# Performance work log

Measured on AMD Instinct MI355X. Metric: run time of the kernel, lower is better.

The kernel has to match this reference:

```python
import jax, jax.numpy as jnp
import numpy as np

B, T, D, H, FF, TB = 4, 512, 768, 12, 3072, 64
DK = D // H
E = float(np.e)
NEG = -1e9  # stand-in for float('-inf') masked_fill; rows always have valid entries


def layer_norm(x, g, b, eps=1e-5):
    m = jnp.mean(x, axis=-1, keepdims=True)
    v = jnp.mean((x - m) ** 2, axis=-1, keepdims=True)
    return (x - m) * jax.lax.rsqrt(v + eps) * g + b


def setup_inputs() -> dict:
    key = jax.random.key(0)
    ks = jax.random.split(key, 20)
    s = 0.02
    w = lambda k, shape: jax.random.normal(k, shape, jnp.float32) * s
    return {
        "x": jax.random.normal(ks[0], (B, T, D), jnp.float32),
        "batch_temporal_mat": jax.random.uniform(ks[1], (B, T, T), jnp.float32, 0.0, 100.0),
        "padding_masks": jnp.ones((B, 1, T, T), jnp.int32),
        # attention linears (stored (in,out): y = x @ W + b, equals torch x @ W_t.T + b)
        "wq": w(ks[2], (D, D)), "bq": w(ks[3], (D,)),
        "wk": w(ks[4], (D, D)), "bk": w(ks[5], (D,)),
        "wv": w(ks[6], (D, D)), "bv": w(ks[7], (D,)),
        "wp": w(ks[8], (D, D)), "bp": w(ks[9], (D,)),
        # temporal-bias MLP: Linear(1,TB) -> leaky_relu(0.2) -> Linear(TB,1)
        "tb1_w": w(ks[10], (1, TB)), "tb1_b": w(ks[11], (TB,)),
        "tb2_w": w(ks[12], (TB, 1)), "tb2_b": w(ks[13], (1,)),
        # FFN
        "fc1_w": w(ks[14], (D, FF)), "fc1_b": w(ks[15], (FF,)),
        "fc2_w": w(ks[16], (FF, D)), "fc2_b": w(ks[17], (D,)),
        # layernorms
        "ln1_g": jnp.ones((D,), jnp.float32), "ln1_b": jnp.zeros((D,), jnp.float32),
        "ln2_g": jnp.ones((D,), jnp.float32), "ln2_b": jnp.zeros((D,), jnp.float32),
    }


def _block(x, batch_temporal_mat, padding_masks,
           wq, bq, wk, bk, wv, bv, wp, bp,
           tb1_w, tb1_b, tb2_w, tb2_b,
           fc1_w, fc1_b, fc2_w, fc2_b,
           ln1_g, ln1_b, ln2_g, ln2_b):
    # pre-LN attention sublayer
    h = layer_norm(x, ln1_g, ln1_b)
    q = (h @ wq + bq).reshape(B, T, H, DK).transpose(0, 2, 1, 3)  # (B,H,T,DK)
    k = (h @ wk + bk).reshape(B, T, H, DK).transpose(0, 2, 1, 3)
    v = (h @ wv + bv).reshape(B, T, H, DK).transpose(0, 2, 1, 3)
    scores = jnp.einsum('bhid,bhjd->bhij', q, k) * (DK ** -0.5)  # (B,H,T,T)

    # temporal bias: 1/log(e + dt), then per-(i,j) MLP with leaky_relu(0.2)
    tm = 1.0 / jnp.log(E + batch_temporal_mat)                    # (B,T,T)
    hb = jax.nn.leaky_relu(tm[..., None] @ tb1_w + tb1_b, 0.2)    # (B,T,T,TB)
    bias = (hb @ tb2_w + tb2_b)[..., 0]                           # (B,T,T)
    scores = scores + bias[:, None]

    # padding mask then causal (future) mask with CLS row 0 fully visible
    scores = jnp.where(padding_masks == 0, NEG, scores)
    causal = jnp.triu(jnp.ones((T, T), bool), 1).at[0, :].set(False)
    scores = jnp.where(causal, NEG, scores)

    p = jax.nn.softmax(scores, axis=-1)
    out = jnp.einsum('bhij,bhjd->bhid', p, v).transpose(0, 2, 1, 3).reshape(B, T, D)
    out = out @ wp + bp
    x = x + out

    # pre-LN FFN sublayer (exact GELU as in nn.GELU default)
    h2 = layer_norm(x, ln2_g, ln2_b)
    m = jax.nn.gelu(h2 @ fc1_w + fc1_b, approximate=False) @ fc2_w + fc2_b
    return x + m


def reference(x, batch_temporal_mat, padding_masks,
              wq, bq, wk, bk, wv, bv, wp, bp,
              tb1_w, tb1_b, tb2_w, tb2_b,
              fc1_w, fc1_b, fc2_w, fc2_b,
              ln1_g, ln1_b, ln2_g, ln2_b):
    return _block(x, batch_temporal_mat, padding_masks,
                  wq, bq, wk, bk, wv, bv, wp, bp,
                  tb1_w, tb1_b, tb2_w, tb2_b,
                  fc1_w, fc1_b, fc2_w, fc2_b,
                  ln1_g, ln1_b, ln2_g, ln2_b)
```

## Files before the change

kernel.cpp:

```cpp
#include <hip/hip_runtime.h>
#include <hip/hip_bf16.h>
#include <math.h>

#define B_ 4
#define T_ 512
#define D_ 768
#define H_ 12
#define FF_ 3072
#define DK_ 64
#define NTOK (B_*T_)
#define NEGV -1e9f

typedef unsigned short u16;
typedef __bf16 bfx8 __attribute__((ext_vector_type(8)));
typedef float f32x4 __attribute__((ext_vector_type(4)));
typedef u16 u16x8 __attribute__((ext_vector_type(8)));

__device__ __forceinline__ u16 f2bf(float f) {
  union { float f; unsigned u; } v; v.f = f;
  unsigned r = (v.u + 0x7FFFu + ((v.u >> 16) & 1u)) >> 16;
  return (u16)r;
}

__device__ __forceinline__ void glds16(const u16* g, u16* l) {
  __builtin_amdgcn_global_load_lds((const __attribute__((address_space(1))) void*)g,
                                   (__attribute__((address_space(3))) void*)l, 16, 0, 0);
}

__global__ __launch_bounds__(256) void prep_kernel(
    const float* __restrict__ x,
    const float* __restrict__ wq, const float* __restrict__ wk,
    const float* __restrict__ wv, const float* __restrict__ wp,
    const float* __restrict__ fc1, const float* __restrict__ fc2,
    u16* wqT, u16* wkT, u16* wvT, u16* wpT, u16* fc1T, u16* fc2T,
    const float* __restrict__ ln1g, const float* __restrict__ ln1b, u16* __restrict__ hbuf,
    const float* __restrict__ tmat, const int* __restrict__ pad,
    const float* __restrict__ tb1w, const float* __restrict__ tb1b,
    const float* __restrict__ tb2w, const float* __restrict__ tb2b,
    float* __restrict__ biasM)
{
  const int bid = blockIdx.x;
  const int tid = threadIdx.x;
  if (bid < 6912) {
    __shared__ float tile[32][33];
    const float* in; u16* outp; int K, N, local;
    if (bid < 2304) {
      int m = bid / 576; local = bid % 576; K = 768; N = 768;
      in   = m == 0 ? wq  : (m == 1 ? wk  : (m == 2 ? wv  : wp));
      outp = m == 0 ? wqT : (m == 1 ? wkT : (m == 2 ? wvT : wpT));
    } else if (bid < 4608) {
      local = bid - 2304; K = 768; N = 3072; in = fc1; outp = fc1T;
    } else {
      local = bid - 4608; K = 3072; N = 768; in = fc2; outp = fc2T;
    }
    const int nt = N / 32;
    const int n0 = (local % nt) * 32, k0 = (local / nt) * 32;
    const int tx = tid & 31, ty = tid >> 5;
    #pragma unroll
    for (int i = 0; i < 4; ++i) {
      int r = ty + i * 8;
      tile[r][tx] = in[(size_t)(k0 + r) * N + n0 + tx];
    }
    __syncthreads();
    #pragma unroll
    for (int i = 0; i < 4; ++i) {
      int r = ty + i * 8;
      outp[(size_t)(n0 + r) * K + k0 + tx] = f2bf(tile[tx][r]);
    }
  } else if (bid < 8960) {
    const int row = bid - 6912;
    const float* xr = x + (size_t)row * D_;
    float v0 = xr[tid], v1 = xr[tid + 256], v2 = xr[tid + 512];
    float s = v0 + v1 + v2;
    float sq = v0 * v0 + v1 * v1 + v2 * v2;
    #pragma unroll
    for (int o = 32; o > 0; o >>= 1) { s += __shfl_down(s, o); sq += __shfl_down(sq, o); }
    __shared__ float ss[4], s2[4];
    int w = tid >> 6;
    if ((tid & 63) == 0) { ss[w] = s; s2[w] = sq; }
    __syncthreads();
    s = ss[0] + ss[1] + ss[2] + ss[3];
    sq = s2[0] + s2[1] + s2[2] + s2[3];
    float mean = s * (1.0f / 768.0f);
    float inv = rsqrtf(sq * (1.0f / 768.0f) - mean * mean + 1e-5f);
    u16* orow = hbuf + (size_t)row * D_;
    orow[tid]       = f2bf((v0 - mean) * inv * ln1g[tid]       + ln1b[tid]);
    orow[tid + 256] = f2bf((v1 - mean) * inv * ln1g[tid + 256] + ln1b[tid + 256]);
    orow[tid + 512] = f2bf((v2 - mean) * inv * ln1g[tid + 512] + ln1b[tid + 512]);
  } else {
    __shared__ float sw1[64], sb1[64], sw2[64];
    if (tid < 64) {
      sw1[tid] = tb1w[tid];
      sb1[tid] = tb1b[tid];
      sw2[tid] = tb2w[tid];
    }
    __syncthreads();
    size_t idx = (size_t)(bid - 8960) * 256 + tid;
    float tm = 1.0f / __logf(2.718281828459045f + tmat[idx]);
    float acc = tb2b[0];
    #pragma unroll
    for (int t = 0; t < 64; ++t) {
      float u = fmaf(tm, sw1[t], sb1[t]);
      u = u > 0.0f ? u : 0.2f * u;
      acc = fmaf(u, sw2[t], acc);
    }
    biasM[idx] = (pad[idx] == 0) ? NEGV : acc;
  }
}

__device__ __forceinline__ void gemm_tile_p2(
    const u16* __restrict__ A, const u16* __restrict__ BT,
    int K, int nk, int m0, int n0,
    u16* As, u16* Bs, f32x4 acc[4][4])
{
  const int tid = threadIdx.x;
  const int w = tid >> 6, lane = tid & 63;
  const int lr = lane & 15, lk = (lane >> 4) * 8;
  const int wm = (w >> 1) * 64, wn = (w & 1) * 64;
  const int c0 = w * 64 + lane, c1 = 256 + c0;
  const int r0 = c0 >> 2, o0 = (c0 & 3) * 8;
  const int r1 = c1 >> 2, o1 = (c1 & 3) * 8;
  const u16* gA0 = A  + (size_t)(m0 + r0) * K + o0;
  const u16* gA1 = A  + (size_t)(m0 + r1) * K + o1;
  const u16* gB0 = BT + (size_t)(n0 + r0) * K + o0;
  const u16* gB1 = BT + (size_t)(n0 + r1) * K + o1;
  u16* la0 = As + w * 512;
  u16* la1 = As + 2048 + w * 512;
  u16* lb0 = Bs + w * 512;
  u16* lb1 = Bs + 2048 + w * 512;
#define ISSUE_TILE(kk, b) do { \
    glds16(gA0 + (size_t)(kk) * 32, la0 + (b) * 4096); \
    glds16(gA1 + (size_t)(kk) * 32, la1 + (b) * 4096); \
    glds16(gB0 + (size_t)(kk) * 32, lb0 + (b) * 4096); \
    glds16(gB1 + (size_t)(kk) * 32, lb1 + (b) * 4096); } while (0)
  ISSUE_TILE(0, 0);
  if (nk > 1) ISSUE_TILE(1, 1);
  int cb = 0;
  for (int kt = 0; kt < nk; ++kt) {
    if (kt < nk - 2) asm volatile("s_waitcnt vmcnt(4)" ::: "memory");
    else             asm volatile("s_waitcnt vmcnt(0)" ::: "memory");
    __builtin_amdgcn_sched_barrier(0);
    __builtin_amdgcn_s_barrier();
    __builtin_amdgcn_sched_barrier(0);
    const u16* Asc = As + cb * 4096;
    const u16* Bsc = Bs + cb * 4096;
    bfx8 af[4], bfr[4];
    #pragma unroll
    for (int t = 0; t < 4; ++t) {
      af[t]  = *(const bfx8*)&Asc[(wm + t * 16 + lr) * 32 + lk];
      bfr[t] = *(const bfx8*)&Bsc[(wn + t * 16 + lr) * 32 + lk];
    }
    #pragma unroll
    for (int rt = 0; rt < 4; ++rt)
      #pragma unroll
      for (int ct = 0; ct < 4; ++ct)
        acc[rt][ct] = __builtin_amdgcn_mfma_f32_16x16x32_bf16(af[rt], bfr[ct], acc[rt][ct], 0, 0, 0);
    if (kt + 2 < nk) {
      int nb = cb + 2; if (nb >= 3) nb -= 3;
      ISSUE_TILE(kt + 2, nb);
    }
    cb = cb + 1; if (cb >= 3) cb = 0;
  }
#undef ISSUE_TILE
}

__global__ __launch_bounds__(256) void gemm_qkv(
    const u16* __restrict__ A,
    const u16* __restrict__ wqT, const u16* __restrict__ wkT, const u16* __restrict__ wvT,
    const float* __restrict__ bq, const float* __restrict__ bk, const float* __restrict__ bv,
    u16* __restrict__ qo, u16* __restrict__ ko, u16* __restrict__ vo)
{
  __shared__ u16 As[3 * 128 * 32];
  __shared__ u16 Bs[3 * 128 * 32];
  const int z = blockIdx.z;
  const u16* BT = z == 0 ? wqT : (z == 1 ? wkT : wvT);
  const float* bias = z == 0 ? bq : (z == 1 ? bk : bv);
  u16* outp = z == 0 ? qo : (z == 1 ? ko : vo);
  const float scale = z == 0 ? 0.125f : 1.0f;
  const int m0 = blockIdx.y * 128, n0 = blockIdx.x * 128;
  f32x4 acc[4][4];
  #pragma unroll
  for (int a = 0; a < 4; ++a)
    #pragma unroll
    for (int bb = 0; bb < 4; ++bb) acc[a][bb] = (f32x4){0.f, 0.f, 0.f, 0.f};
  gemm_tile_p2(A, BT, D_, D_ / 32, m0, n0, As, Bs, acc);
  const int tid = threadIdx.x;
  const int w = tid >> 6, lane = tid & 63;
  const int lr = lane & 15;
  const int wm = (w >> 1) * 64, wn = (w & 1) * 64;
  #pragma unroll
  for (int rt = 0; rt < 4; ++rt)
    #pragma unroll
    for (int ct = 0; ct < 4; ++ct)
      #pragma unroll
      for (int r = 0; r < 4; ++r) {
        int m = m0 + wm + rt * 16 + (lane >> 4) * 4 + r;
        int n = n0 + wn + ct * 16 + lr;
        float val = (acc[rt][ct][r] + bias[n]) * scale;
        int b = m >> 9, t = m & 511, hh = n >> 6, d = n & 63;
        if (z < 2) outp[(((size_t)b * H_ + hh) * T_ + t) * DK_ + d] = f2bf(val);
        else       outp[(((size_t)b * H_ + hh) * DK_ + d) * T_ + t] = f2bf(val);
      }
}

__global__ __launch_bounds__(256) void gemm_res(
    const u16* __restrict__ A, const u16* __restrict__ BT,
    const float* __restrict__ bias, const float* __restrict__ resid,
    float* __restrict__ outp, int K)
{
  __shared__ u16 As[3 * 128 * 32];
  __shared__ u16 Bs[3 * 64 * 32];
  const int bid = blockIdx.x;
  const int xcd = bid & 7, i = bid >> 3;
  const int mt = xcd * 2 + (i >= 12 ? 1 : 0);
  const int nt = i - (i >= 12 ? 12 : 0);
  const int m0 = mt * 128, n0 = nt * 64;
  const int nk = K / 32;

  const int tid = threadIdx.x;
  const int w = tid >> 6, lane = tid & 63;
  const int lr = lane & 15, hi = lane >> 4, lk = hi * 8;
  const int wm = (w >> 1) * 64, wn = (w & 1) * 32;
  const int c0 = w * 64 + lane, c1 = 256 + c0;
  const int rA0 = c0 >> 2, oA0 = (c0 & 3) * 8;
  const int rA1 = c1 >> 2, oA1 = (c1 & 3) * 8;
  const int rB  = c0 >> 2, oB  = (c0 & 3) * 8;
  const u16* gA0 = A  + (size_t)(m0 + rA0) * K + oA0;
  const u16* gA1 = A  + (size_t)(m0 + rA1) * K + oA1;
  const u16* gB  = BT + (size_t)(n0 + rB) * K + oB;
  u16* la0 = As + w * 512;
  u16* la1 = As + 2048 + w * 512;
  u16* lb  = Bs + w * 512;

  f32x4 acc[4][2];
  #pragma unroll
  for (int a = 0; a < 4; ++a)
    #pragma unroll
    for (int bb = 0; bb < 2; ++bb) acc[a][bb] = (f32x4){0.f, 0.f, 0.f, 0.f};

#define ISSUE_T(kk, b) do { \
    glds16(gA0 + (size_t)(kk) * 32, la0 + (b) * 4096); \
    glds16(gA1 + (size_t)(kk) * 32, la1 + (b) * 4096); \
    glds16(gB  + (size_t)(kk) * 32, lb  + (b) * 2048); } while (0)
  ISSUE_T(0, 0);
  if (nk > 1) ISSUE_T(1, 1);
  int cb = 0;
  for (int kt = 0; kt < nk; ++kt) {
    if (kt < nk - 2) asm volatile("s_waitcnt vmcnt(3)" ::: "memory");
    else             asm volatile("s_waitcnt vmcnt(0)" ::: "memory");
    __builtin_amdgcn_sched_barrier(0);
    __builtin_amdgcn_s_barrier();
    __builtin_amdgcn_sched_barrier(0);
    const u16* Asc = As + cb * 4096;
    const u16* Bsc = Bs + cb * 2048;
    bfx8 af[4], bfr[2];
    #pragma unroll
    for (int t = 0; t < 4; ++t)
      af[t] = *(const bfx8*)&Asc[(wm + t * 16 + lr) * 32 + lk];
    #pragma unroll
    for (int u = 0; u < 2; ++u)
      bfr[u] = *(const bfx8*)&Bsc[(wn + u * 16 + lr) * 32 + lk];
    #pragma unroll
    for (int rt = 0; rt < 4; ++rt)
      #pragma unroll
      for (int ct = 0; ct < 2; ++ct)
        acc[rt][ct] = __builtin_amdgcn_mfma_f32_16x16x32_bf16(af[rt], bfr[ct], acc[rt][ct], 0, 0, 0);
    if (kt + 2 < nk) {
      int nb = cb + 2; if (nb >= 3) nb -= 3;
      ISSUE_T(kt + 2, nb);
    }
    cb = cb + 1; if (cb >= 3) cb = 0;
  }
#undef ISSUE_T

  #pragma unroll
  for (int rt = 0; rt < 4; ++rt)
    #pragma unroll
    for (int ct = 0; ct < 2; ++ct)
      #pragma unroll
      for (int r = 0; r < 4; ++r) {
        int m = m0 + wm + rt * 16 + hi * 4 + r;
        int n = n0 + wn + ct * 16 + lr;
        size_t off = (size_t)m * D_ + n;
        outp[off] = acc[rt][ct][r] + bias[n] + resid[off];
      }
}

__global__ __launch_bounds__(256) void gemm_gelu(
    const u16* __restrict__ A, const u16* __restrict__ BT,
    const float* __restrict__ bias, u16* __restrict__ outp, int M, int N, int K)
{
  __shared__ u16 As[3 * 128 * 32];
  __shared__ u16 Bs[3 * 128 * 32];
  const int m0 = blockIdx.y * 128, n0 = blockIdx.x * 128;
  f32x4 acc[4][4];
  #pragma unroll
  for (int a = 0; a < 4; ++a)
    #pragma unroll
    for (int bb = 0; bb < 4; ++bb) acc[a][bb] = (f32x4){0.f, 0.f, 0.f, 0.f};
  gemm_tile_p2(A, BT, K, K / 32, m0, n0, As, Bs, acc);
  const int tid = threadIdx.x;
  const int w = tid >> 6, lane = tid & 63;
  const int lr = lane & 15;
  const int wm = (w >> 1) * 64, wn = (w & 1) * 64;
  #pragma unroll
  for (int rt = 0; rt < 4; ++rt)
    #pragma unroll
    for (int ct = 0; ct < 4; ++ct)
      #pragma unroll
      for (int r = 0; r < 4; ++r) {
        int m = m0 + wm + rt * 16 + (lane >> 4) * 4 + r;
        int n = n0 + wn + ct * 16 + lr;
        float val = acc[rt][ct][r] + bias[n];
        float gl = 0.5f * val * (1.0f + erff(val * 0.7071067811865475f));
        outp[(size_t)m * N + n] = f2bf(gl);
      }
}

__global__ __launch_bounds__(256) void ln2_kernel(
    const float* __restrict__ x1, const float* __restrict__ g, const float* __restrict__ bta,
    u16* __restrict__ h2)
{
  const int row = blockIdx.x;
  const int tid = threadIdx.x;
  const size_t base = (size_t)row * D_;
  float v[3];
  float s = 0.f, sq = 0.f;
  #pragma unroll
  for (int i = 0; i < 3; ++i) {
    int c = tid + i * 256;
    float val = x1[base + c];
    v[i] = val;
    s += val; sq += val * val;
  }
  #pragma unroll
  for (int o = 32; o > 0; o >>= 1) { s += __shfl_down(s, o); sq += __shfl_down(sq, o); }
  __shared__ float ss[4], s2[4];
  int w = tid >> 6;
  if ((tid & 63) == 0) { ss[w] = s; s2[w] = sq; }
  __syncthreads();
  s = ss[0] + ss[1] + ss[2] + ss[3];
  sq = s2[0] + s2[1] + s2[2] + s2[3];
  float mean = s * (1.0f / 768.0f);
  float inv = rsqrtf(sq * (1.0f / 768.0f) - mean * mean + 1e-5f);
  #pragma unroll
  for (int i = 0; i < 3; ++i) {
    int c = tid + i * 256;
    h2[base + c] = f2bf((v[i] - mean) * inv * g[c] + bta[c]);
  }
}

__global__ __launch_bounds__(256) void attn_kernel(
    const u16* __restrict__ q, const u16* __restrict__ k, const u16* __restrict__ vT,
    const float* __restrict__ biasM, u16* __restrict__ ao)
{
  __shared__ u16 P[32 * 512];
  __shared__ float pmax[128], psum[128];
  const int tid = threadIdx.x;
  const int w = tid >> 6, lane = tid & 63;
  const int lr = lane & 15, hi = lane >> 4, lk = hi * 8;

  const int bid = blockIdx.x;
  const int xcd = bid & 7, idx = bid >> 3;
  const int bh = xcd * 6 + (idx >> 4);
  const int i0 = (idx & 15) * 32;
  const int b = bh / H_, h = bh % H_;
  const int tmax = (i0 == 0) ? 31 : ((i0 >> 4) + 1);
  const int nks  = (i0 == 0) ? 16 : ((i0 >> 5) + 1);

  bfx8 qf[2][2];
  #pragma unroll
  for (int g = 0; g < 2; ++g)
    #pragma unroll
    for (int ks = 0; ks < 2; ++ks)
      qf[g][ks] = *(const bfx8*)(q + ((size_t)bh * T_ + i0 + g * 16 + lr) * DK_ + ks * 32 + lk);
  f32x4 acc[8][2];
  float mx[2][4];
  #pragma unroll
  for (int g = 0; g < 2; ++g)
    #pragma unroll
    for (int r = 0; r < 4; ++r) mx[g][r] = -3.4e38f;
  #pragma unroll
  for (int ct = 0; ct < 8; ++ct) {
    const int t = ct * 4 + w;
    if (t > tmax) continue;
    const int j0 = t * 16;
    bfx8 kf0 = *(const bfx8*)(k + ((size_t)bh * T_ + j0 + lr) * DK_ + lk);
    bfx8 kf1 = *(const bfx8*)(k + ((size_t)bh * T_ + j0 + lr) * DK_ + 32 + lk);
    const int j = j0 + lr;
    #pragma unroll
    for (int g = 0; g < 2; ++g) {
      f32x4 a0 = (f32x4){0.f, 0.f, 0.f, 0.f};
      a0 = __builtin_amdgcn_mfma_f32_16x16x32_bf16(qf[g][0], kf0, a0, 0, 0, 0);
      a0 = __builtin_amdgcn_mfma_f32_16x16x32_bf16(qf[g][1], kf1, a0, 0, 0, 0);
      #pragma unroll
      for (int r = 0; r < 4; ++r) {
        int i = i0 + g * 16 + hi * 4 + r;
        float s = a0[r] + biasM[((size_t)b * T_ + i) * T_ + j];
        if (j > i && i != 0) s = NEGV;
        a0[r] = s;
        mx[g][r] = fmaxf(mx[g][r], s);
      }
      acc[ct][g] = a0;
    }
  }
  #pragma unroll
  for (int o = 1; o < 16; o <<= 1)
    #pragma unroll
    for (int g = 0; g < 2; ++g)
      #pragma unroll
      for (int r = 0; r < 4; ++r) mx[g][r] = fmaxf(mx[g][r], __shfl_xor(mx[g][r], o));
  if (lr == 0) {
    #pragma unroll
    for (int g = 0; g < 2; ++g)
      #pragma unroll
      for (int r = 0; r < 4; ++r) pmax[w * 32 + g * 16 + hi * 4 + r] = mx[g][r];
  }
  __syncthreads();

  float M2[2][4], sm[2][4];
  #pragma unroll
  for (int g = 0; g < 2; ++g)
    #pragma unroll
    for (int r = 0; r < 4; ++r) {
      int row = g * 16 + hi * 4 + r;
      M2[g][r] = fmaxf(fmaxf(pmax[row], pmax[32 + row]), fmaxf(pmax[64 + row], pmax[96 + row]));
      sm[g][r] = 0.f;
    }
  char* Pb = (char*)P;
  #pragma unroll
  for (int ct = 0; ct < 8; ++ct) {
    const int t = ct * 4 + w;
    if (t > tmax) continue;
    const int col = t * 16 + lr;
    #pragma unroll
    for (int g = 0; g < 2; ++g)
      #pragma unroll
      for (int r = 0; r < 4; ++r) {
        float pexp = __expf(acc[ct][g][r] - M2[g][r]);
        sm[g][r] += pexp;
        int row = g * 16 + hi * 4 + r;
        int byte = (row * 1024 + col * 2) ^ ((row & 7) << 4);
        *(u16*)(Pb + byte) = f2bf(pexp);
      }
  }
  #pragma unroll
  for (int o = 1; o < 16; o <<= 1)
    #pragma unroll
    for (int g = 0; g < 2; ++g)
      #pragma unroll
      for (int r = 0; r < 4; ++r) sm[g][r] += __shfl_xor(sm[g][r], o);
  if (lr == 0) {
    #pragma unroll
    for (int g = 0; g < 2; ++g)
      #pragma unroll
      for (int r = 0; r < 4; ++r) psum[w * 32 + g * 16 + hi * 4 + r] = sm[g][r];
  }
  __syncthreads();

  float rinv[2][4];
  #pragma unroll
  for (int g = 0; g < 2; ++g)
    #pragma unroll
    for (int r = 0; r < 4; ++r) {
      int row = g * 16 + hi * 4 + r;
      rinv[g][r] = 1.0f / (psum[row] + psum[32 + row] + psum[64 + row] + psum[96 + row]);
    }

  {
    const int n0 = w * 16;
    f32x4 oa0 = (f32x4){0.f, 0.f, 0.f, 0.f};
    f32x4 oa1 = (f32x4){0.f, 0.f, 0.f, 0.f};
    for (int ks = 0; ks < nks; ++ks) {
      bfx8 vf = *(const bfx8*)(vT + ((size_t)bh * DK_ + n0 + lr) * T_ + ks * 32 + lk);
      int byte0 = (lr * 1024 + (ks * 32 + lk) * 2) ^ ((lr & 7) << 4);
      int byte1 = ((16 + lr) * 1024 + (ks * 32 + lk) * 2) ^ ((lr & 7) << 4);
      bfx8 pa0 = *(const bfx8*)(Pb + byte0);
      bfx8 pa1 = *(const bfx8*)(Pb + byte1);
      oa0 = __builtin_amdgcn_mfma_f32_16x16x32_bf16(pa0, vf, oa0, 0, 0, 0);
      oa1 = __builtin_amdgcn_mfma_f32_16x16x32_bf16(pa1, vf, oa1, 0, 0, 0);
    }
    #pragma unroll
    for (int r = 0; r < 4; ++r) {
      int i = i0 + hi * 4 + r;
      ao[((size_t)b * T_ + i) * D_ + h * DK_ + n0 + lr] = f2bf(oa0[r] * rinv[0][r]);
    }
    #pragma unroll
    for (int r = 0; r < 4; ++r) {
      int i = i0 + 16 + hi * 4 + r;
      ao[((size_t)b * T_ + i) * D_ + h * DK_ + n0 + lr] = f2bf(oa1[r] * rinv[1][r]);
    }
  }
}

extern "C" void kernel_launch(void* const* d_in, const int* in_sizes, int n_in,
                              void* d_out, int out_size, void* d_ws, size_t ws_size,
                              hipStream_t stream) {
  (void)in_sizes; (void)n_in; (void)out_size; (void)ws_size;
  const float* x    = (const float*)d_in[0];
  const float* tmat = (const float*)d_in[1];
  const int*   pad  = (const int*)d_in[2];
  const float* wq = (const float*)d_in[3];  const float* bq = (const float*)d_in[4];
  const float* wk = (const float*)d_in[5];  const float* bk = (const float*)d_in[6];
  const float* wv = (const float*)d_in[7];  const float* bv = (const float*)d_in[8];
  const float* wp = (const float*)d_in[9];  const float* bp = (const float*)d_in[10];
  const float* tb1w = (const float*)d_in[11]; const float* tb1b = (const float*)d_in[12];
  const float* tb2w = (const float*)d_in[13]; const float* tb2b = (const float*)d_in[14];
  const float* fc1w = (const float*)d_in[15]; const float* fc1b = (const float*)d_in[16];
  const float* fc2w = (const float*)d_in[17]; const float* fc2b = (const float*)d_in[18];
  const float* ln1g = (const float*)d_in[19]; const float* ln1b = (const float*)d_in[20];
  const float* ln2g = (const float*)d_in[21]; const float* ln2b = (const float*)d_in[22];
  float* out = (float*)d_out;

  char* p = (char*)d_ws;
  u16* wqT  = (u16*)p; p += (size_t)768 * 768 * 2;
  u16* wkT  = (u16*)p; p += (size_t)768 * 768 * 2;
  u16* wvT  = (u16*)p; p += (size_t)768 * 768 * 2;
  u16* wpT  = (u16*)p; p += (size_t)768 * 768 * 2;
  u16* fc1T = (u16*)p; p += (size_t)768 * 3072 * 2;
  u16* fc2T = (u16*)p; p += (size_t)3072 * 768 * 2;
  float* x1 = (float*)p; p += (size_t)NTOK * D_ * 4;
  u16* gbuf = (u16*)p; p += (size_t)NTOK * FF_ * 2;
  u16* hbuf = (u16*)p; p += (size_t)NTOK * D_ * 2;
  u16* qb   = (u16*)p; p += (size_t)NTOK * D_ * 2;
  u16* kb   = (u16*)p; p += (size_t)NTOK * D_ * 2;
  u16* vTb  = (u16*)p; p += (size_t)NTOK * D_ * 2;
  float* biasM = (float*)p; p += (size_t)B_ * T_ * T_ * 4;
  u16* ao   = (u16*)p; p += (size_t)NTOK * D_ * 2;
  u16* h2   = (u16*)p; p += (size_t)NTOK * D_ * 2;

  prep_kernel<<<13056, 256, 0, stream>>>(x, wq, wk, wv, wp, fc1w, fc2w,
                                         wqT, wkT, wvT, wpT, fc1T, fc2T,
                                         ln1g, ln1b, hbuf,
                                         tmat, pad, tb1w, tb1b, tb2w, tb2b, biasM);

  gemm_qkv<<<dim3(6, 16, 3), 256, 0, stream>>>(hbuf, wqT, wkT, wvT, bq, bk, bv, qb, kb, vTb);
  attn_kernel<<<768, 256, 0, stream>>>(qb, kb, vTb, biasM, ao);

  gemm_res<<<192, 256, 0, stream>>>(ao, wpT, bp, x, x1, 768);
  ln2_kernel<<<NTOK, 256, 0, stream>>>(x1, ln2g, ln2b, h2);

  gemm_gelu<<<dim3(24, 16), 256, 0, stream>>>(h2, fc1T, fc1b, gbuf, NTOK, FF_, 768);

  gemm_res<<<192, 256, 0, stream>>>(gbuf, fc2T, fc2b, x1, out, 3072);
}
```

Measured before the change: 151.1 us.

## Split-K the FC2 GEMM with bf16 partials and a separate reduce kernel

Replaces the 192-block fused FC2 GEMM plus residual with an 8-way split-K GEMM (768 blocks of 128x128 tiles) that writes bf16 partial sums. A new elementwise reduce kernel then adds the partials, bias and residual. The aim is to fill more compute units on the long-K (3072) GEMM. In exchange it adds an extra launch and about 25 MB of partial-buffer traffic, and rounding the partials to bf16 loses precision.

```diff
diff --git a/kernel.cpp b/kernel.cpp
--- a/kernel.cpp
+++ b/kernel.cpp
@@ -20,6 +20,10 @@
   union { float f; unsigned u; } v; v.f = f;
   unsigned r = (v.u + 0x7FFFu + ((v.u >> 16) & 1u)) >> 16;
   return (u16)r;
+}
+
+__device__ __forceinline__ float bf2f(u16 u) {
+  union { unsigned u; float f; } c; c.u = (unsigned)u << 16; return c.f;
 }
 
 __device__ __forceinline__ void glds16(const u16* g, u16* l) {
@@ -110,7 +114,7 @@
 
 __device__ __forceinline__ void gemm_tile_p2(
     const u16* __restrict__ A, const u16* __restrict__ BT,
-    int K, int nk, int m0, int n0,
+    int K, int nk, int m0, int n0, int k0,
     u16* As, u16* Bs, f32x4 acc[4][4])
 {
   const int tid = threadIdx.x;
@@ -120,10 +124,10 @@
   const int c0 = w * 64 + lane, c1 = 256 + c0;
   const int r0 = c0 >> 2, o0 = (c0 & 3) * 8;
   const int r1 = c1 >> 2, o1 = (c1 & 3) * 8;
-  const u16* gA0 = A  + (size_t)(m0 + r0) * K + o0;
-  const u16* gA1 = A  + (size_t)(m0 + r1) * K + o1;
-  const u16* gB0 = BT + (size_t)(n0 + r0) * K + o0;
-  const u16* gB1 = BT + (size_t)(n0 + r1) * K + o1;
+  const u16* gA0 = A  + (size_t)(m0 + r0) * K + k0 + o0;
+  const u16* gA1 = A  + (size_t)(m0 + r1) * K + k0 + o1;
+  const u16* gB0 = BT + (size_t)(n0 + r0) * K + k0 + o0;
+  const u16* gB1 = BT + (size_t)(n0 + r1) * K + k0 + o1;
   u16* la0 = As + w * 512;
   u16* la1 = As + 2048 + w * 512;
   u16* lb0 = Bs + w * 512;
@@ -183,7 +187,7 @@
   for (int a = 0; a < 4; ++a)
     #pragma unroll
     for (int bb = 0; bb < 4; ++bb) acc[a][bb] = (f32x4){0.f, 0.f, 0.f, 0.f};
-  gemm_tile_p2(A, BT, D_, D_ / 32, m0, n0, As, Bs, acc);
+  gemm_tile_p2(A, BT, D_, D_ / 32, m0, n0, 0, As, Bs, acc);
   const int tid = threadIdx.x;
   const int w = tid >> 6, lane = tid & 63;
   const int lr = lane & 15;
@@ -286,6 +290,63 @@
       }
 }
 
+__global__ __launch_bounds__(256) void gemm_part_bf16(
+    const u16* __restrict__ A, const u16* __restrict__ BT,
+    u16* __restrict__ part, int M, int N, int K, int Ksplit)
+{
+  __shared__ u16 As[3 * 128 * 32];
+  __shared__ u16 Bs[3 * 128 * 32];
+  const int m0 = blockIdx.y * 128, n0 = blockIdx.x * 128;
+  const int kz = blockIdx.z;
+  f32x4 acc[4][4];
+  #pragma unroll
+  for (int a = 0; a < 4; ++a)
+    #pragma unroll
+    for (int bb = 0; bb < 4; ++bb) acc[a][bb] = (f32x4){0.f, 0.f, 0.f, 0.f};
+  gemm_tile_p2(A, BT, K, Ksplit / 32, m0, n0, kz * Ksplit, As, Bs, acc);
+  const int tid = threadIdx.x;
+  const int w = tid >> 6, lane = tid & 63;
+  const int lr = lane & 15;
+  const int wm = (w >> 1) * 64, wn = (w & 1) * 64;
+  u16* pp = part + (size_t)kz * M * N;
+  #pragma unroll
+  for (int rt = 0; rt < 4; ++rt)
+    #pragma unroll
+    for (int ct = 0; ct < 4; ++ct)
+      #pragma unroll
+      for (int r = 0; r < 4; ++r) {
+        int m = m0 + wm + rt * 16 + (lane >> 4) * 4 + r;
+        int n = n0 + wn + ct * 16 + lr;
+        pp[(size_t)m * N + n] = f2bf(acc[rt][ct][r]);
+      }
+}
+
+__global__ __launch_bounds__(256) void reduce_out(
+    const u16* __restrict__ part, const float* __restrict__ x1,
+    const float* __restrict__ bias, float* __restrict__ out)
+{
+  const size_t base = ((size_t)blockIdx.x * 256 + threadIdx.x) * 8;
+  const size_t slab = (size_t)NTOK * D_;
+  const int nb = (int)(base % D_);
+  float s[8];
+  float4 a0 = *(const float4*)&x1[base];
+  float4 a1 = *(const float4*)&x1[base + 4];
+  float4 b0 = *(const float4*)&bias[nb];
+  float4 b1 = *(const float4*)&bias[nb + 4];
+  s[0] = a0.x + b0.x; s[1] = a0.y + b0.y; s[2] = a0.z + b0.z; s[3] = a0.w + b0.w;
+  s[4] = a1.x + b1.x; s[5] = a1.y + b1.y; s[6] = a1.z + b1.z; s[7] = a1.w + b1.w;
+  #pragma unroll
+  for (int kz = 0; kz < 8; ++kz) {
+    u16x8 pv = *(const u16x8*)&part[kz * slab + base];
+    #pragma unroll
+    for (int j = 0; j < 8; ++j) s[j] += bf2f(pv[j]);
+  }
+  float4 o0 = {s[0], s[1], s[2], s[3]};
+  float4 o1 = {s[4], s[5], s[6], s[7]};
+  *(float4*)&out[base]     = o0;
+  *(float4*)&out[base + 4] = o1;
+}
+
 __global__ __launch_bounds__(256) void gemm_gelu(
     const u16* __restrict__ A, const u16* __restrict__ BT,
     const float* __restrict__ bias, u16* __restrict__ outp, int M, int N, int K)
@@ -298,7 +359,7 @@
   for (int a = 0; a < 4; ++a)
     #pragma unroll
     for (int bb = 0; bb < 4; ++bb) acc[a][bb] = (f32x4){0.f, 0.f, 0.f, 0.f};
-  gemm_tile_p2(A, BT, K, K / 32, m0, n0, As, Bs, acc);
+  gemm_tile_p2(A, BT, K, K / 32, m0, n0, 0, As, Bs, acc);
   const int tid = threadIdx.x;
   const int w = tid >> 6, lane = tid & 63;
   const int lr = lane & 15;
@@ -528,6 +589,7 @@
   float* biasM = (float*)p; p += (size_t)B_ * T_ * T_ * 4;
   u16* ao   = (u16*)p; p += (size_t)NTOK * D_ * 2;
   u16* h2   = (u16*)p; p += (size_t)NTOK * D_ * 2;
+  u16* partF = (u16*)p; p += (size_t)8 * NTOK * D_ * 2;
 
   prep_kernel<<<13056, 256, 0, stream>>>(x, wq, wk, wv, wp, fc1w, fc2w,
                                          wqT, wkT, wvT, wpT, fc1T, fc2T,
@@ -542,5 +604,6 @@
 
   gemm_gelu<<<dim3(24, 16), 256, 0, stream>>>(h2, fc1T, fc1b, gbuf, NTOK, FF_, 768);
 
-  gemm_res<<<192, 256, 0, stream>>>(gbuf, fc2T, fc2b, x1, out, 3072);
-}
+  gemm_part_bf16<<<dim3(6, 16, 8), 256, 0, stream>>>(gbuf, fc2T, partF, NTOK, 768, 3072, 384);
+  reduce_out<<<NTOK * D_ / 8 / 256, 256, 0, stream>>>(partF, x1, fc2b, out);
+}
```

Result: faster. 136.8 us (-9.4%).
